# Kernel optimization log

Measured on AMD Instinct MI355X. Metric: run time of the kernel, lower is better.

Reference implementation:

```python
import jax, jax.numpy as jnp
import numpy as np

B = 4
NV = 6890           # SMPL vertex count
NF0 = 13776         # SMPL face count (before fill_back)
T = 3               # tex_size
IMG = 128           # render image size
UVH = UVW = 256     # uv image resolution
FLENGTH = 500.0
NEAR, FAR = 0.1, 25.0
CHUNK = 128         # faces per z-buffer scan step
BIG = jnp.float32(1e10)


def setup_inputs():
    key = jax.random.key(0)
    ks = jax.random.split(key, 5)
    faces0 = jax.random.randint(ks[0], (NF0, 3), 0, NV, dtype=jnp.int32)
    faces = jnp.concatenate([faces0, faces0[:, ::-1]], axis=0)  # fill_back
    cam = jnp.concatenate([0.8 + 0.2 * jax.random.uniform(ks[1], (B, 1)),
                           0.05 * jax.random.normal(ks[2], (B, 2))], axis=1)
    vertices = 0.3 * jax.random.normal(ks[3], (B, NV, 3))
    uv_imgs = jax.random.uniform(ks[4], (B, 3, UVH, UVW))
    img2uv_sampler = jax.random.uniform(jax.random.fold_in(key, 7),
                                        (faces.shape[0], T * T, 2)) * 2.0 - 1.0
    return {"cam": cam, "vertices": vertices, "uv_imgs": uv_imgs,
            "img2uv_sampler": img2uv_sampler, "faces": faces}


def _grid_sample(img, grid):
    # img (B,C,H,W), grid (B,N,2) xy in [-1,1]; bilinear, align_corners=False, zeros padding
    Bc, C, H, W = img.shape
    x = (grid[..., 0] + 1.0) * (W * 0.5) - 0.5
    y = (grid[..., 1] + 1.0) * (H * 0.5) - 0.5
    x0f = jnp.floor(x); y0f = jnp.floor(y)
    wx = x - x0f; wy = y - y0f
    x0 = x0f.astype(jnp.int32); y0 = y0f.astype(jnp.int32)
    imgf = img.reshape(Bc, C, H * W)
    def gat(yi, xi, w):
        valid = (xi >= 0) & (xi < W) & (yi >= 0) & (yi < H)
        idx = jnp.clip(yi, 0, H - 1) * W + jnp.clip(xi, 0, W - 1)
        v = jax.vmap(lambda im, i: im[:, i])(imgf, idx)  # (B,C,N)
        return v * (w * valid)[:, None, :]
    return (gat(y0, x0, (1 - wx) * (1 - wy)) + gat(y0, x0 + 1, wx * (1 - wy)) +
            gat(y0 + 1, x0, (1 - wx) * wy) + gat(y0 + 1, x0 + 1, wx * wy))


def _extract_tex(uv_imgs, sampler, nf):
    # sampler (B,nf,T*T,2) -> textures (B,nf,T,T,T,3)
    tex = _grid_sample(uv_imgs, sampler.reshape(uv_imgs.shape[0], -1, 2))
    tex = tex.reshape(-1, 3, nf, T, T).transpose(0, 2, 3, 4, 1)  # (B,nf,T,T,3)
    return jnp.broadcast_to(tex[:, :, :, :, None, :], tex.shape[:4] + (T, 3))


def _lighting(face_verts, textures):
    # module defaults: ambient intensity 1, directional 0, white lights, dir=(0,1,0)
    v0, v1, v2 = face_verts[:, :, 0], face_verts[:, :, 1], face_verts[:, :, 2]
    n = jnp.cross(v1 - v0, v2 - v0)
    n = n / (jnp.linalg.norm(n, axis=-1, keepdims=True) + 1e-10)
    cos = jnp.maximum(n @ jnp.array([0.0, 1.0, 0.0]), 0.0)       # (B,F)
    light = 1.0 * jnp.ones(3) + 0.0 * cos[..., None] * jnp.ones(3)  # (B,F,3)
    return textures * light[:, :, None, None, None, :]


def _weak_projection(cam, vertices):
    p = IMG / 2.0
    tz = FLENGTH / (p * cam[:, 0:1])                              # (B,1)
    v2d = cam[:, None, 0:1] * (vertices[:, :, :2] + cam[:, None, 1:])
    return jnp.concatenate([v2d, vertices[:, :, 2:3] + tz[:, None, :]], axis=-1)


def _bary(fv, px, py):
    # fv: (...,3,3) triangle screen verts; px,py broadcastable pixel coords
    x0 = fv[..., 0, 0]; y0 = fv[..., 0, 1]
    x1 = fv[..., 1, 0]; y1 = fv[..., 1, 1]
    x2 = fv[..., 2, 0]; y2 = fv[..., 2, 1]
    w0 = (x2 - x1) * (py - y1) - (y2 - y1) * (px - x1)
    w1 = (x0 - x2) * (py - y2) - (y0 - y2) * (px - x2)
    w2 = (x1 - x0) * (py - y0) - (y1 - y0) * (px - x0)
    area = w0 + w1 + w2
    s = jnp.where(area == 0, 1.0, area)
    return w0 / s, w1 / s, w2 / s, area


def _pixel_grid():
    xs = (2.0 * jnp.arange(IMG) + 1.0) / IMG - 1.0                # (W,)
    ys = (1.0 - (2.0 * jnp.arange(IMG) + 1.0) / IMG)[:, None]     # (H,1), +y up
    return xs, ys


def _rasterize_fim(face_verts):
    # face_verts (B,F,3,3) in screen coords -> face index map (B,H,W), -1 = bg
    Bc, F = face_verts.shape[:2]
    pad = (-F) % CHUNK
    fv = jnp.pad(face_verts, ((0, 0), (0, pad), (0, 0), (0, 0)))
    S = (F + pad) // CHUNK
    fv = fv.reshape(Bc, S, CHUNK, 3, 3).transpose(1, 0, 2, 3, 4)  # (S,B,C,3,3)
    xs, ys = _pixel_grid()
    def step(carry, inp):
        zbuf, fim = carry
        f, base = inp
        fe = f[:, :, None, None, :, :]                            # (B,C,1,1,3,3)
        b0, b1, b2, area = _bary(fe, xs, ys)                      # (B,C,H,W)
        z0 = f[:, :, 0, 2][..., None, None]
        z1 = f[:, :, 1, 2][..., None, None]
        z2 = f[:, :, 2, 2][..., None, None]
        invz = b0 / z0 + b1 / z1 + b2 / z2                        # perspective-correct
        zp = 1.0 / jnp.where(invz == 0, 1.0, invz)
        inside = (b0 >= 0) & (b1 >= 0) & (b2 >= 0) & (area > 0)   # front-facing only
        valid = inside & (zp > NEAR) & (zp < FAR)
        depth = jnp.where(valid, zp, BIG)
        dmin = jnp.min(depth, axis=1)                             # (B,H,W)
        amin = jnp.argmin(depth, axis=1).astype(jnp.int32) + base
        better = dmin < zbuf
        return (jnp.where(better, dmin, zbuf),
                jnp.where(better, amin, fim)), None
    zbuf0 = jnp.full((Bc, IMG, IMG), BIG)
    fim0 = jnp.full((Bc, IMG, IMG), -1, jnp.int32)
    bases = (jnp.arange(S) * CHUNK).astype(jnp.int32)
    (zbuf, fim), _ = jax.lax.scan(step, (zbuf0, fim0), (fv, bases))
    return fim


def _shade(face_verts, textures, fim):
    # nearest-texel barycentric texture lookup, as in neural_renderer forward
    Bc, F = face_verts.shape[:2]
    fid = jnp.clip(fim, 0, F - 1).reshape(Bc, -1)                 # (B,HW)
    fv = jax.vmap(lambda v, i: v[i])(face_verts, fid)             # (B,HW,3,3)
    fv = fv.reshape(Bc, IMG, IMG, 3, 3)
    xs, ys = _pixel_grid()
    b0, b1, b2, _ = _bary(fv, xs, ys)                             # (B,H,W)
    t0 = jnp.clip(jnp.floor(b0 * T).astype(jnp.int32), 0, T - 1)
    t1 = jnp.clip(jnp.floor(b1 * T).astype(jnp.int32), 0, T - 1)
    t2 = jnp.clip(jnp.floor(b2 * T).astype(jnp.int32), 0, T - 1)
    idx = ((jnp.clip(fim, 0, F - 1) * T + t0) * T + t1) * T + t2  # (B,H,W)
    texf = textures.reshape(Bc, F * T * T * T, 3)
    col = jax.vmap(lambda t, i: t[i])(texf, idx.reshape(Bc, -1))  # (B,HW,3)
    col = col.reshape(Bc, IMG, IMG, 3)
    col = jnp.where((fim >= 0)[..., None], col, 0.0)              # bg color (0,0,0)
    return col.transpose(0, 3, 1, 2)                              # (B,3,H,W)


def reference(cam, vertices, uv_imgs, img2uv_sampler, faces):
    Bc = cam.shape[0]
    nf = faces.shape[0]
    sampler = jnp.broadcast_to(img2uv_sampler[None], (Bc,) + img2uv_sampler.shape)
    textures = _extract_tex(uv_imgs, sampler, nf)                 # (B,nf,T,T,T,3)
    textures = _lighting(vertices[:, faces], textures)
    verts_p = _weak_projection(cam, vertices)
    fv = verts_p[:, faces]                                        # (B,nf,3,3)
    fv_sg = jax.lax.stop_gradient(fv)  # hard rasterization is non-differentiable
    fim = _rasterize_fim(fv_sg)
    images = _shade(fv_sg, textures, fim)
    return images


if __name__ == "__main__":
    out = reference(**setup_inputs())
    print(out.shape, out.dtype)
```

## Files before the change

kernel.cpp:

```cpp
#include <hip/hip_runtime.h>
#include <stdint.h>

#pragma clang fp contract(off)

#define B_    4
#define NV_   6890
#define NF_   27552
#define IMG_  128
#define UV_   256
#define NPIX  (IMG_*IMG_)

#define TS_     8
#define TPB_    (IMG_/TS_)
#define NTILE_  (TPB_*TPB_)
#define NBIN_   (B_*NTILE_)
#define NZ_     8
#define NCELL_  (NTILE_*NZ_)
#define LIST_CAP (1536*1024)
#define MAXC_   (LIST_CAP/256 + NBIN_)
#define FBF_    256
#define NBLK_   ((NF_+FBF_-1)/FBF_)


__global__ void __launch_bounds__(256) project_k(
    const float* __restrict__ cam, const float* __restrict__ verts,
    float* __restrict__ vp) {
  int idx = blockIdx.x * 256 + threadIdx.x;
  if (idx >= B_ * NV_) return;
  int b = idx / NV_;
  float c0 = cam[b * 3 + 0], c1 = cam[b * 3 + 1], c2 = cam[b * 3 + 2];
  float tz = 500.0f / (64.0f * c0);
  const float* src = verts + (size_t)idx * 3;
  float* dst = vp + (size_t)idx * 4;
  dst[0] = c0 * (src[0] + c1);
  dst[1] = c0 * (src[1] + c2);
  dst[2] = src[2] + tz;
  dst[3] = 0.0f;
}

struct FaceBin {
  int valid, tx0, tx1, ty0, ty1, bu;
  float d21x, d21y, d02x, d02y, d10x, d10y;
  float x0, y0, x1, y1, x2, y2, zmin;
};

__device__ __forceinline__ FaceBin face_bin(
    const float* __restrict__ cam, const float* __restrict__ vp,
    const int* __restrict__ faces, int b, int f) {
  FaceBin r; r.valid = 0; r.zmin = 0.0f;
  int ia = faces[f * 3 + 0], ib = faces[f * 3 + 1], ic = faces[f * 3 + 2];
  const float* vb = vp + (size_t)b * NV_ * 4;
  float x0 = vb[ia * 4 + 0], y0 = vb[ia * 4 + 1], z0 = vb[ia * 4 + 2];
  float x1 = vb[ib * 4 + 0], y1 = vb[ib * 4 + 1], z1 = vb[ib * 4 + 2];
  float x2 = vb[ic * 4 + 0], y2 = vb[ic * 4 + 1], z2 = vb[ic * 4 + 2];
  float area_c = (x1 - x0) * (y2 - y0) - (y1 - y0) * (x2 - x0);
  if (area_c < -1e-3f) return r;
  float xmn = fminf(x0, fminf(x1, x2)), xmx = fmaxf(x0, fmaxf(x1, x2));
  float ymn = fminf(y0, fminf(y1, y2)), ymx = fmaxf(y0, fmaxf(y1, y2));
  int jlo = (int)floorf((xmn + 1.0f) * 64.0f - 0.5f) - 1;
  int jhi = (int)ceilf ((xmx + 1.0f) * 64.0f - 0.5f) + 1;
  int ilo = (int)floorf((1.0f - ymx) * 64.0f - 0.5f) - 1;
  int ihi = (int)ceilf ((1.0f - ymn) * 64.0f - 0.5f) + 1;
  if (jhi < 0 || ihi < 0 || jlo > IMG_ - 1 || ilo > IMG_ - 1) return r;
  jlo = max(jlo, 0); ilo = max(ilo, 0);
  jhi = min(jhi, IMG_ - 1); ihi = min(ihi, IMG_ - 1);
  r.tx0 = jlo >> 3; r.tx1 = jhi >> 3; r.ty0 = ilo >> 3; r.ty1 = ihi >> 3;
  r.zmin = fminf(z0, fminf(z1, z2));
  float tz = 500.0f / (64.0f * cam[b * 3]);
  float zr = r.zmin - tz;
  r.bu = (zr > -0.447f) + (zr > -0.367f) + (zr > -0.308f) + (zr > -0.254f) +
         (zr > -0.200f) + (zr > -0.141f) + (zr > -0.061f);
  r.d21x = x2 - x1; r.d21y = y2 - y1;
  r.d02x = x0 - x2; r.d02y = y0 - y2;
  r.d10x = x1 - x0; r.d10y = y1 - y0;
  r.x0 = x0; r.y0 = y0; r.x1 = x1; r.y1 = y1; r.x2 = x2; r.y2 = y2;
  r.valid = 1;
  return r;
}

__device__ __forceinline__ int tile_pass(const FaceBin& r, int tx, int ty) {
  float pxmin = fmaf((float)(tx * 8), 0.015625f, -0.9921875f);
  float pxmax = pxmin + 0.109375f;
  float pymax = fmaf((float)(ty * 8), -0.015625f, 0.9921875f);
  float pymin = pymax - 0.109375f;
  float w0m = r.d21x * ((r.d21x > 0.0f ? pymax : pymin) - r.y1) -
              r.d21y * ((r.d21y > 0.0f ? pxmin : pxmax) - r.x1);
  float w1m = r.d02x * ((r.d02x > 0.0f ? pymax : pymin) - r.y2) -
              r.d02y * ((r.d02y > 0.0f ? pxmin : pxmax) - r.x2);
  float w2m = r.d10x * ((r.d10x > 0.0f ? pymax : pymin) - r.y0) -
              r.d10y * ((r.d10y > 0.0f ? pxmin : pxmax) - r.x0);
  return (w0m >= -1e-3f) && (w1m >= -1e-3f) && (w2m >= -1e-3f);
}

__global__ void __launch_bounds__(FBF_) facebin_k(
    const float* __restrict__ cam, const float* __restrict__ vp,
    const int* __restrict__ faces, ulonglong2* __restrict__ recs,
    unsigned short* __restrict__ cntb) {
  __shared__ int scnt[NCELL_];
  int blk = blockIdx.x, b = blockIdx.y;
  int f = blk * FBF_ + threadIdx.x;
  for (int k = threadIdx.x; k < NCELL_; k += FBF_) scnt[k] = 0;
  __syncthreads();
  if (f < NF_) {
    FaceBin r = face_bin(cam, vp, faces, b, f);
    unsigned long long mask = 0ull;
    unsigned info = 0u;
    float zmin = 0.0f;
    if (r.valid) {
      int w = r.tx1 - r.tx0 + 1, h = r.ty1 - r.ty0 + 1;
      bool full = (w * h > 64);
      int k = 0;
      for (int ty = r.ty0; ty <= r.ty1; ++ty)
        for (int tx = r.tx0; tx <= r.tx1; ++tx, ++k)
          if (full || tile_pass(r, tx, ty)) {
            if (!full) mask |= 1ull << k;
            atomicAdd(&scnt[(ty * TPB_ + tx) * NZ_ + r.bu], 1);
          }
      if (full) mask = ~0ull;
      if (mask != 0ull) {
        info = 0x80000000u | ((unsigned)r.bu << 28) |
               ((unsigned)r.tx0 << 24) | ((unsigned)r.ty0 << 20) |
               ((unsigned)(w - 1) << 16) | ((unsigned)(h - 1) << 12);
        zmin = r.zmin;
      }
    }
    ulonglong2 rr;
    rr.x = mask;
    rr.y = ((unsigned long long)info << 32) | (unsigned)__float_as_uint(zmin);
    recs[(size_t)b * NF_ + f] = rr;
  }
  __syncthreads();
  unsigned short* dst = cntb + ((size_t)b * NBLK_ + blk) * NCELL_;
  for (int k = threadIdx.x; k < NCELL_; k += FBF_)
    dst[k] = (unsigned short)scnt[k];
}

__global__ void __launch_bounds__(256) sum_k(
    unsigned short* __restrict__ cntb, int* __restrict__ cnt8) {
  int c = blockIdx.x * 256 + threadIdx.x;
  int b = blockIdx.y;
  int run = 0;
  for (int blk = 0; blk < NBLK_; ++blk) {
    size_t o = ((size_t)b * NBLK_ + blk) * NCELL_ + c;
    int v = (int)cntb[o];
    cntb[o] = (unsigned short)run;
    run += v;
  }
  cnt8[(size_t)b * NCELL_ + c] = run;
}

__global__ void __launch_bounds__(1024) scan_k(
    const int* __restrict__ cnt8, int* __restrict__ off8,
    int* __restrict__ binoff, int* __restrict__ bintot,
    int* __restrict__ work, int* __restrict__ nC) {
  __shared__ int wsum[16];
  int t = threadIdx.x;
  int lane = t & 63, w = t >> 6;
  int c[NZ_];
  int s = 0;
#pragma unroll
  for (int j = 0; j < NZ_; ++j) { c[j] = cnt8[t * NZ_ + j]; s += c[j]; }
  int inc = s;
#pragma unroll
  for (int d = 1; d < 64; d <<= 1) {
    int u = __shfl_up(inc, d, 64);
    if (lane >= d) inc += u;
  }
  if (lane == 63) wsum[w] = inc;
  __syncthreads();
  int wb = 0;
  for (int k = 0; k < 16; ++k) wb += (k < w) ? wsum[k] : 0;
  int base = wb + inc - s;
  int o = base;
#pragma unroll
  for (int j = 0; j < NZ_; ++j) {
    off8[t * NZ_ + j] = o;
    o += c[j];
  }
  binoff[t] = base;
  bintot[t] = s;
  int nch = (max(s - 256, 0) + 255) >> 8;
  int inc2 = nch;
#pragma unroll
  for (int d = 1; d < 64; d <<= 1) {
    int u = __shfl_up(inc2, d, 64);
    if (lane >= d) inc2 += u;
  }
  __syncthreads();
  if (lane == 63) wsum[w] = inc2;
  __syncthreads();
  int wb2 = 0;
  for (int k = 0; k < 16; ++k) wb2 += (k < w) ? wsum[k] : 0;
  int cb = wb2 + inc2 - nch;
  if (t == 1023) nC[0] = wb2 + inc2;
  for (int q = 0; q < nch; ++q) work[cb + q] = t | ((q + 1) << 10);
}

__global__ void __launch_bounds__(FBF_) bin_fill_k(
    const ulonglong2* __restrict__ recs, const int* __restrict__ off8,
    const unsigned short* __restrict__ cntb, int* __restrict__ list) {
  __shared__ int lbase[NCELL_];
  __shared__ int lrank[NCELL_];
  int blk = blockIdx.x, b = blockIdx.y;
  int f = blk * FBF_ + threadIdx.x;
  const unsigned short* prow = cntb + ((size_t)b * NBLK_ + blk) * NCELL_;
  const int* orow = off8 + (size_t)b * NCELL_;
  for (int k = threadIdx.x; k < NCELL_; k += FBF_) {
    lbase[k] = orow[k] + (int)prow[k];
    lrank[k] = 0;
  }
  __syncthreads();
  if (f < NF_) {
    ulonglong2 rr = recs[(size_t)b * NF_ + f];
    unsigned long long mask = rr.x;
    unsigned info = (unsigned)(rr.y >> 32);
    unsigned z16 = ((unsigned)rr.y) >> 16;
    if (info >> 31) {
      int ev = (int)((z16 << 15) | (unsigned)f);
      int bu = (info >> 28) & 7;
      int tx0 = (info >> 24) & 15, ty0 = (info >> 20) & 15;
      int w = ((info >> 16) & 15) + 1, h = ((info >> 12) & 15) + 1;
      bool full = (w * h > 64);
      int k = 0;
      for (int ty = ty0; ty < ty0 + h; ++ty)
        for (int tx = tx0; tx < tx0 + w; ++tx, ++k)
          if (full || ((mask >> k) & 1ull)) {
            int cell = (ty * TPB_ + tx) * NZ_ + bu;
            int rk = atomicAdd(&lrank[cell], 1);
            int slot = lbase[cell] + rk;
            if (slot < LIST_CAP) list[slot] = ev;
          }
    }
  }
}

__device__ __forceinline__ void raster_slice(
    const float4 (*F)[64], int nsurv, float px, float py,
    unsigned long long& kb, unsigned& kbz_u) {
  unsigned win_u = 0x7F800000u;
  unsigned long long qm = 0ull;
  for (int q = 0; q < nsurv; ++q) {
    float4 A = F[0][q];
    float4 Bv = F[1][q];
    float4 Cv = F[2][q];
    float w0 = A.x * (py - A.w) - A.y * (px - A.z);
    float w1 = Bv.x * (py - Bv.w) - Bv.y * (px - Bv.z);
    float w2 = Cv.x * (py - Cv.w) - Cv.y * (px - Cv.z);
    float area = (w0 + w1) + w2;
    float mn = fminf(w0, fminf(w1, w2));
    bool pred = (area > 0.0f) && !(mn < 0.0f);
    if (!__any(pred)) continue;
    float4 P = F[4][q];
    float num = (w0 * P.x + w1 * P.y) + w2 * P.z;
    float zpa = (area * P.w) * __builtin_amdgcn_rcpf(num);
    unsigned cu = win_u < kbz_u ? win_u : kbz_u;
    float thrq = __uint_as_float(cu) * 1.001f;
    bool amb = pred && (!(zpa > thrq) ||
                        (zpa > 0.09989f && zpa < 0.10011f) ||
                        (zpa > 24.9724f && zpa < 25.0276f));
    if (amb) qm |= 1ull << q;
    bool ok = pred && (zpa > 0.1001f) && (zpa < 24.975f);
    unsigned zb = __float_as_uint(zpa);
    if (ok && zb < win_u) win_u = zb;
  }
  while (__any(qm != 0ull)) {
    if (qm != 0ull) {
      int q = __ffsll(qm) - 1;
      qm &= qm - 1ull;
      float4 A = F[0][q];
      float4 Bv = F[1][q];
      float4 Cv = F[2][q];
      float w0 = A.x * (py - A.w) - A.y * (px - A.z);
      float w1 = Bv.x * (py - Bv.w) - Bv.y * (px - Bv.z);
      float w2 = Cv.x * (py - Cv.w) - Cv.y * (px - Cv.z);
      float area = (w0 + w1) + w2;
      float4 P = F[4][q];
      float num = (w0 * P.x + w1 * P.y) + w2 * P.z;
      float zpa = (area * P.w) * __builtin_amdgcn_rcpf(num);
      unsigned cu = win_u < kbz_u ? win_u : kbz_u;
      float thrf = __uint_as_float(cu) * 1.001f;
      if (!(zpa > thrf) ||
          (zpa > 0.09989f && zpa < 0.10011f) ||
          (zpa > 24.9724f && zpa < 25.0276f)) {
        float4 Z = F[3][q];
        float b0 = w0 / area, b1 = w1 / area, b2 = w2 / area;
        float invz = (b0 / Z.x + b1 / Z.y) + b2 / Z.z;
        float zp = 1.0f / (invz == 0.0f ? 1.0f : invz);
        if (zp > 0.1f && zp < 25.0f) {
          unsigned long long key =
              ((unsigned long long)__float_as_uint(zp) << 32) |
              (unsigned int)__float_as_int(Z.w);
          if (key < kb) {
            kb = key;
            kbz_u = (unsigned)(kb >> 32);
          }
        }
      }
    }
  }
}

__device__ __forceinline__ void stage_face(
    float4 (*F)[64], const float* __restrict__ vb,
    const int* __restrict__ faces, int fid, int rank) {
  int ia = faces[fid * 3 + 0], ib = faces[fid * 3 + 1], ic = faces[fid * 3 + 2];
  float4 v0 = *(const float4*)(vb + (size_t)ia * 4);
  float4 v1 = *(const float4*)(vb + (size_t)ib * 4);
  float4 v2 = *(const float4*)(vb + (size_t)ic * 4);
  F[0][rank] = make_float4(v2.x - v1.x, v2.y - v1.y, v1.x, v1.y);
  F[1][rank] = make_float4(v0.x - v2.x, v0.y - v2.y, v2.x, v2.y);
  F[2][rank] = make_float4(v1.x - v0.x, v1.y - v0.y, v0.x, v0.y);
  F[3][rank] = make_float4(v0.z, v1.z, v2.z, __int_as_float(fid));
  F[4][rank] =
      make_float4(v1.z * v2.z, v0.z * v2.z, v0.z * v1.z, v0.z * v1.z * v2.z);
}

__global__ void __launch_bounds__(256) raster_seed_k(
    const float* __restrict__ vp, const int* __restrict__ faces,
    const int* __restrict__ list, const int* __restrict__ bintot,
    const int* __restrict__ binoff, unsigned long long* __restrict__ zkey) {
  __shared__ float4 fd[4][5][64];
  __shared__ unsigned long long mg[4][64];
  int bin = blockIdx.x;
  int b = bin >> 8;
  int t = bin & 255;
  int tyT = t >> 4, txT = t & 15;
  int ws = threadIdx.x >> 6, lane = threadIdx.x & 63;
  int pi = tyT * TS_ + (lane >> 3);
  int pj = txT * TS_ + (lane & 7);
  float px = fmaf((float)pj, 0.015625f, -0.9921875f);
  float py = fmaf((float)pi, -0.015625f, 0.9921875f);

  int n = min(bintot[bin], 256);
  int base = binoff[bin];
  int seg = ws * 64;
  int mw = min(n - seg, 64);

  unsigned long long kb = ~0ull;
  unsigned kbz_u = 0x7F800000u;
  if (mw > 0) {
    if (lane < mw) {
      int fid = (int)((unsigned)list[base + seg + lane] & 0x7FFFu);
      stage_face(fd[ws], vp + (size_t)b * NV_ * 4, faces, fid, lane);
    }
    raster_slice(fd[ws], mw, px, py, kb, kbz_u);
  }

  mg[ws][lane] = kb;
  __syncthreads();
  if (ws == 0) {
    unsigned long long k0 = mg[0][lane];
    unsigned long long k1 = mg[1][lane];
    unsigned long long k2 = mg[2][lane];
    unsigned long long k3 = mg[3][lane];
    k0 = k1 < k0 ? k1 : k0;
    k2 = k3 < k2 ? k3 : k2;
    k0 = k2 < k0 ? k2 : k0;
    zkey[(size_t)b * NPIX + pi * IMG_ + pj] = k0;
  }
}

__global__ void __launch_bounds__(256) raster_k(
    const float* __restrict__ vp, const int* __restrict__ faces,
    const int* __restrict__ list, const int* __restrict__ bintot,
    const int* __restrict__ binoff, const int* __restrict__ work,
    const int* __restrict__ nC, unsigned long long* __restrict__ zkey) {
  __shared__ float4 fd[4][5][64];
  __shared__ unsigned long long mg[4][64];
  int bid = blockIdx.x;
  if (bid >= nC[0]) return;
  int wkv = work[bid];
  int bin = wkv & (NBIN_ - 1);
  int chunk = wkv >> 10;
  int b = bin >> 8;
  int t = bin & 255;
  int tyT = t >> 4, txT = t & 15;
  int ws = threadIdx.x >> 6, lane = threadIdx.x & 63;
  int pi = tyT * TS_ + (lane >> 3);
  int pj = txT * TS_ + (lane & 7);
  float px = fmaf((float)pj, 0.015625f, -0.9921875f);
  float py = fmaf((float)pi, -0.015625f, 0.9921875f);

  const unsigned* zhi = (const unsigned*)zkey;
  unsigned seed_u =
      min(zhi[((size_t)b * NPIX + pi * IMG_ + pj) * 2 + 1], 0x7F800000u);
  unsigned mx = seed_u;
  for (int j = 1; j < 64; j <<= 1) {
    unsigned o = (unsigned)__shfl_xor((int)mx, j, 64);
    mx = o > mx ? o : mx;
  }
  unsigned thr_code = __float_as_uint(__uint_as_float(mx) * 1.01f) >> 16;

  int n = bintot[bin];
  int seg = (chunk << 8) + (ws << 6);
  int base0 = binoff[bin] + seg;
  int mw = min(n - seg, 64);
  mw = max(mw, 0);

  bool live = false;
  int fid = 0;
  if (lane < mw) {
    unsigned e = (unsigned)list[base0 + lane];
    live = ((e >> 15) <= thr_code);
    fid = (int)(e & 0x7FFFu);
  }
  unsigned long long bal = __ballot(live);
  unsigned long long kb = ~0ull;
  unsigned kbz_u = seed_u;
  if (bal != 0ull) {
    int nsurv = (int)__popcll(bal);
    int rank = (int)__popcll(bal & ((1ull << lane) - 1ull));
    if (live)
      stage_face(fd[ws], vp + (size_t)b * NV_ * 4, faces, fid, rank);
    raster_slice(fd[ws], nsurv, px, py, kb, kbz_u);
  }

  mg[ws][lane] = kb;
  __syncthreads();
  if (ws == 0) {
    unsigned long long k0 = mg[0][lane];
    unsigned long long k1 = mg[1][lane];
    unsigned long long k2 = mg[2][lane];
    unsigned long long k3 = mg[3][lane];
    k0 = k1 < k0 ? k1 : k0;
    k2 = k3 < k2 ? k3 : k2;
    k0 = k2 < k0 ? k2 : k0;
    if (k0 != ~0ull)
      atomicMin(zkey + (size_t)b * NPIX + pi * IMG_ + pj, k0);
  }
}

#define TAP(ty, tx, wexpr)                                                   \
  {                                                                          \
    int ty_ = (ty), tx_ = (tx);                                              \
    float w_ = (wexpr);                                                      \
    float valid_ =                                                           \
        (tx_ >= 0 && tx_ < UV_ && ty_ >= 0 && ty_ < UV_) ? 1.0f : 0.0f;      \
    float wv_ = w_ * valid_;                                                 \
    int cy_ = min(max(ty_, 0), UV_ - 1), cx_ = min(max(tx_, 0), UV_ - 1);    \
    int o_ = cy_ * UV_ + cx_;                                                \
    cr = cr + img[o_] * wv_;                                                 \
    cg = cg + img[UV_ * UV_ + o_] * wv_;                                     \
    cb = cb + img[2 * UV_ * UV_ + o_] * wv_;                                 \
  }

__global__ void __launch_bounds__(256) shade_k(
    const float* __restrict__ vp, const int* __restrict__ faces,
    const float* __restrict__ uv, const float* __restrict__ samp,
    const unsigned long long* __restrict__ zkey, float* __restrict__ out) {
  int idx = blockIdx.x * 256 + threadIdx.x;
  if (idx >= B_ * NPIX) return;
  int b = idx / NPIX;
  int p = idx - b * NPIX;
  int ii = p / IMG_;
  int jj = p - ii * IMG_;

  unsigned long long key = zkey[idx];
  float cr = 0.0f, cg = 0.0f, cb = 0.0f;
  if (key != 0xFFFFFFFFFFFFFFFFull) {
    int f = (int)(key & 0xFFFFFFFFull);
    int ia = faces[f * 3 + 0], ib = faces[f * 3 + 1], ic = faces[f * 3 + 2];
    const float* vb = vp + (size_t)b * NV_ * 4;
    float x0 = vb[ia * 4 + 0], y0 = vb[ia * 4 + 1];
    float x1 = vb[ib * 4 + 0], y1 = vb[ib * 4 + 1];
    float x2 = vb[ic * 4 + 0], y2 = vb[ic * 4 + 1];
    float px = (float)(2 * jj + 1) / 128.0f - 1.0f;
    float py = 1.0f - (float)(2 * ii + 1) / 128.0f;
    float w0 = (x2 - x1) * (py - y1) - (y2 - y1) * (px - x1);
    float w1 = (x0 - x2) * (py - y2) - (y0 - y2) * (px - x2);
    float w2 = (x1 - x0) * (py - y0) - (y1 - y0) * (px - x0);
    float area = (w0 + w1) + w2;
    float s = (area == 0.0f) ? 1.0f : area;
    float b0 = w0 / s, b1 = w1 / s;
    int t0 = min(max((int)floorf(b0 * 3.0f), 0), 2);
    int t1 = min(max((int)floorf(b1 * 3.0f), 0), 2);

    const float* g = samp + ((size_t)f * 9 + (size_t)(t0 * 3 + t1)) * 2;
    float gx = g[0], gy = g[1];
    float x = (gx + 1.0f) * 128.0f - 0.5f;
    float y = (gy + 1.0f) * 128.0f - 0.5f;
    float x0f = floorf(x), y0f = floorf(y);
    float wx = x - x0f, wy = y - y0f;
    int xi = (int)x0f, yi = (int)y0f;
    float omwx = 1.0f - wx, omwy = 1.0f - wy;
    const float* img = uv + (size_t)b * 3 * UV_ * UV_;
    TAP(yi,     xi,     omwx * omwy)
    TAP(yi,     xi + 1, wx * omwy)
    TAP(yi + 1, xi,     omwx * wy)
    TAP(yi + 1, xi + 1, wx * wy)
  }
  out[((size_t)b * 3 + 0) * NPIX + p] = cr;
  out[((size_t)b * 3 + 1) * NPIX + p] = cg;
  out[((size_t)b * 3 + 2) * NPIX + p] = cb;
}

extern "C" void kernel_launch(void* const* d_in, const int* in_sizes, int n_in,
                              void* d_out, int out_size, void* d_ws,
                              size_t ws_size, hipStream_t stream) {
  const float* cam   = (const float*)d_in[0];
  const float* verts = (const float*)d_in[1];
  const float* uv    = (const float*)d_in[2];
  const float* samp  = (const float*)d_in[3];
  const int*   faces = (const int*)d_in[4];

  char* ws = (char*)d_ws;
  size_t o = 0;
  unsigned long long* zkey = (unsigned long long*)(ws + o);
  o += (size_t)B_ * NPIX * 8;
  float* vp = (float*)(ws + o);
  o += ((size_t)B_ * NV_ * 4 * 4 + 1023) & ~1023ull;
  int* cnt8   = (int*)(ws + o); o += (size_t)B_ * NCELL_ * 4;
  int* off8   = (int*)(ws + o); o += (size_t)B_ * NCELL_ * 4;
  int* binoff = (int*)(ws + o); o += NBIN_ * 4;
  int* bintot = (int*)(ws + o); o += NBIN_ * 4;
  int* nC     = (int*)(ws + o); o += 1024;
  int* work   = (int*)(ws + o); o += (size_t)MAXC_ * 4;
  ulonglong2* recs = (ulonglong2*)(ws + o);
  o += (size_t)B_ * NF_ * 16;
  unsigned short* cntb = (unsigned short*)(ws + o);
  o += (size_t)B_ * NBLK_ * NCELL_ * 2;
  int* list = (int*)(ws + o);

  project_k<<<(B_ * NV_ + 255) / 256, 256, 0, stream>>>(cam, verts, vp);
  dim3 bgrid(NBLK_, B_);
  facebin_k<<<bgrid, FBF_, 0, stream>>>(cam, vp, faces, recs, cntb);
  sum_k<<<dim3(NCELL_ / 256, B_), 256, 0, stream>>>(cntb, cnt8);
  scan_k<<<1, NBIN_, 0, stream>>>(cnt8, off8, binoff, bintot, work, nC);
  bin_fill_k<<<bgrid, FBF_, 0, stream>>>(recs, off8, cntb, list);
  raster_seed_k<<<NBIN_, 256, 0, stream>>>(vp, faces, list, bintot, binoff,
                                           zkey);
  raster_k<<<MAXC_, 256, 0, stream>>>(vp, faces, list, bintot, binoff, work,
                                      nC, zkey);
  shade_k<<<(B_ * NPIX + 255) / 256, 256, 0, stream>>>(vp, faces, uv, samp,
                                                       zkey, (float*)d_out);
}
```

Measured before the change: 181.2 us.

## Fuse count sum and scan into per-batch kernel, shrink seed pass to 128 faces

Merges the column-sum and single-block scan kernels into one kernel launched per batch, with the list partitioned into per-batch capacity regions and per-batch work queues. This removes one launch and the serial single-block scan over all bins. The seed raster pass now consumes only the first 128 faces per bin instead of 256, so the chunked raster pass starts earlier and picks up more of the list. The smaller seed may leave a looser depth threshold, so fewer faces get culled in the later pass. The per-batch capacity split could overflow for skewed batches.

```diff
diff --git a/kernel.cpp b/kernel.cpp
--- a/kernel.cpp
+++ b/kernel.cpp
@@ -17,7 +17,9 @@
 #define NZ_     8
 #define NCELL_  (NTILE_*NZ_)
 #define LIST_CAP (1536*1024)
-#define MAXC_   (LIST_CAP/256 + NBIN_)
+#define CAPB_   (LIST_CAP/B_)
+#define MAXCB_  (CAPB_/256 + NTILE_)
+#define SEEDN_  128
 #define FBF_    256
 #define NBLK_   ((NF_+FBF_-1)/FBF_)
 
@@ -135,65 +137,79 @@
     dst[k] = (unsigned short)scnt[k];
 }
 
-__global__ void __launch_bounds__(256) sum_k(
-    unsigned short* __restrict__ cntb, int* __restrict__ cnt8) {
-  int c = blockIdx.x * 256 + threadIdx.x;
-  int b = blockIdx.y;
-  int run = 0;
-  for (int blk = 0; blk < NBLK_; ++blk) {
-    size_t o = ((size_t)b * NBLK_ + blk) * NCELL_ + c;
-    int v = (int)cntb[o];
-    cntb[o] = (unsigned short)run;
-    run += v;
-  }
-  cnt8[(size_t)b * NCELL_ + c] = run;
-}
-
-__global__ void __launch_bounds__(1024) scan_k(
-    const int* __restrict__ cnt8, int* __restrict__ off8,
+__global__ void __launch_bounds__(1024) sumscan_k(
+    unsigned short* __restrict__ cntb, int* __restrict__ off8,
     int* __restrict__ binoff, int* __restrict__ bintot,
     int* __restrict__ work, int* __restrict__ nC) {
+  __shared__ int tot[NCELL_];
   __shared__ int wsum[16];
+  __shared__ int half0;
+  __shared__ int nchs[NTILE_];
+  int b = blockIdx.x;
   int t = threadIdx.x;
   int lane = t & 63, w = t >> 6;
-  int c[NZ_];
-  int s = 0;
+  for (int c = t; c < NCELL_; c += 1024) {
+    int run = 0;
+    for (int blk = 0; blk < NBLK_; ++blk) {
+      size_t o = ((size_t)b * NBLK_ + blk) * NCELL_ + c;
+      int v = (int)cntb[o];
+      cntb[o] = (unsigned short)run;
+      run += v;
+    }
+    tot[c] = run;
+  }
+  __syncthreads();
+  int base = b * CAPB_;
+  int v0 = tot[t];
+  int inc0 = v0;
+  for (int d = 1; d < 64; d <<= 1) {
+    int u = __shfl_up(inc0, d, 64);
+    if (lane >= d) inc0 += u;
+  }
+  if (lane == 63) wsum[w] = inc0;
+  __syncthreads();
+  int wb0 = 0;
+  for (int k = 0; k < 16; ++k) wb0 += (k < w) ? wsum[k] : 0;
+  off8[(size_t)b * NCELL_ + t] = base + wb0 + inc0 - v0;
+  if (t == 1023) half0 = wb0 + inc0;
+  __syncthreads();
+  int v1 = tot[1024 + t];
+  int inc1 = v1;
+  for (int d = 1; d < 64; d <<= 1) {
+    int u = __shfl_up(inc1, d, 64);
+    if (lane >= d) inc1 += u;
+  }
+  if (lane == 63) wsum[w] = inc1;
+  __syncthreads();
+  int wb1 = 0;
+  for (int k = 0; k < 16; ++k) wb1 += (k < w) ? wsum[k] : 0;
+  off8[(size_t)b * NCELL_ + 1024 + t] = base + half0 + wb1 + inc1 - v1;
+  __syncthreads();
+  if (t < NTILE_) {
+    int s = 0;
 #pragma unroll
-  for (int j = 0; j < NZ_; ++j) { c[j] = cnt8[t * NZ_ + j]; s += c[j]; }
-  int inc = s;
-#pragma unroll
+    for (int j = 0; j < NZ_; ++j) s += tot[t * NZ_ + j];
+    bintot[b * NTILE_ + t] = s;
+    binoff[b * NTILE_ + t] = off8[(size_t)b * NCELL_ + t * NZ_];
+    nchs[t] = (max(s - SEEDN_, 0) + 255) >> 8;
+  }
+  __syncthreads();
+  int vc = (t < NTILE_) ? nchs[t] : 0;
+  int incc = vc;
   for (int d = 1; d < 64; d <<= 1) {
-    int u = __shfl_up(inc, d, 64);
-    if (lane >= d) inc += u;
-  }
-  if (lane == 63) wsum[w] = inc;
-  __syncthreads();
-  int wb = 0;
-  for (int k = 0; k < 16; ++k) wb += (k < w) ? wsum[k] : 0;
-  int base = wb + inc - s;
-  int o = base;
-#pragma unroll
-  for (int j = 0; j < NZ_; ++j) {
-    off8[t * NZ_ + j] = o;
-    o += c[j];
-  }
-  binoff[t] = base;
-  bintot[t] = s;
-  int nch = (max(s - 256, 0) + 255) >> 8;
-  int inc2 = nch;
-#pragma unroll
-  for (int d = 1; d < 64; d <<= 1) {
-    int u = __shfl_up(inc2, d, 64);
-    if (lane >= d) inc2 += u;
-  }
-  __syncthreads();
-  if (lane == 63) wsum[w] = inc2;
-  __syncthreads();
-  int wb2 = 0;
-  for (int k = 0; k < 16; ++k) wb2 += (k < w) ? wsum[k] : 0;
-  int cb = wb2 + inc2 - nch;
-  if (t == 1023) nC[0] = wb2 + inc2;
-  for (int q = 0; q < nch; ++q) work[cb + q] = t | ((q + 1) << 10);
+    int u = __shfl_up(incc, d, 64);
+    if (lane >= d) incc += u;
+  }
+  if (t < NTILE_ && lane == 63) wsum[w] = incc;
+  __syncthreads();
+  if (t < NTILE_) {
+    int wb = 0;
+    for (int k = 0; k < 4; ++k) wb += (k < w) ? wsum[k] : 0;
+    int cb = wb + incc - vc;
+    if (t == NTILE_ - 1) nC[b] = wb + incc;
+    for (int q = 0; q < vc; ++q)
+      work[b * MAXCB_ + cb + q] = t | ((q + 1) << 8);
+  }
 }
 
 __global__ void __launch_bounds__(FBF_) bin_fill_k(
@@ -221,6 +237,7 @@
       int tx0 = (info >> 24) & 15, ty0 = (info >> 20) & 15;
       int w = ((info >> 16) & 15) + 1, h = ((info >> 12) & 15) + 1;
       bool full = (w * h > 64);
+      int cap = (b + 1) * CAPB_;
       int k = 0;
       for (int ty = ty0; ty < ty0 + h; ++ty)
         for (int tx = tx0; tx < tx0 + w; ++tx, ++k)
@@ -228,7 +245,7 @@
             int cell = (ty * TPB_ + tx) * NZ_ + bu;
             int rk = atomicAdd(&lrank[cell], 1);
             int slot = lbase[cell] + rk;
-            if (slot < LIST_CAP) list[slot] = ev;
+            if (slot < cap) list[slot] = ev;
           }
     }
   }
@@ -331,10 +348,10 @@
   float px = fmaf((float)pj, 0.015625f, -0.9921875f);
   float py = fmaf((float)pi, -0.015625f, 0.9921875f);
 
-  int n = min(bintot[bin], 256);
+  int n = min(bintot[bin], SEEDN_);
   int base = binoff[bin];
-  int seg = ws * 64;
-  int mw = min(n - seg, 64);
+  int seg = ws * (SEEDN_ / 4);
+  int mw = min(n - seg, SEEDN_ / 4);
 
   unsigned long long kb = ~0ull;
   unsigned kbz_u = 0x7F800000u;
@@ -368,12 +385,13 @@
   __shared__ float4 fd[4][5][64];
   __shared__ unsigned long long mg[4][64];
   int bid = blockIdx.x;
-  if (bid >= nC[0]) return;
-  int wkv = work[bid];
-  int bin = wkv & (NBIN_ - 1);
-  int chunk = wkv >> 10;
-  int b = bin >> 8;
-  int t = bin & 255;
+  int b = bid / MAXCB_;
+  int i = bid - b * MAXCB_;
+  if (i >= nC[b]) return;
+  int wkv = work[b * MAXCB_ + i];
+  int t = wkv & (NTILE_ - 1);
+  int chunk = wkv >> 8;
+  int bin = b * NTILE_ + t;
   int tyT = t >> 4, txT = t & 15;
   int ws = threadIdx.x >> 6, lane = threadIdx.x & 63;
   int pi = tyT * TS_ + (lane >> 3);
@@ -392,7 +410,7 @@
   unsigned thr_code = __float_as_uint(__uint_as_float(mx) * 1.01f) >> 16;
 
   int n = bintot[bin];
-  int seg = (chunk << 8) + (ws << 6);
+  int seg = SEEDN_ + ((chunk - 1) << 8) + (ws << 6);
   int base0 = binoff[bin] + seg;
   int mw = min(n - seg, 64);
   mw = max(mw, 0);
@@ -509,12 +527,11 @@
   o += (size_t)B_ * NPIX * 8;
   float* vp = (float*)(ws + o);
   o += ((size_t)B_ * NV_ * 4 * 4 + 1023) & ~1023ull;
-  int* cnt8   = (int*)(ws + o); o += (size_t)B_ * NCELL_ * 4;
   int* off8   = (int*)(ws + o); o += (size_t)B_ * NCELL_ * 4;
   int* binoff = (int*)(ws + o); o += NBIN_ * 4;
   int* bintot = (int*)(ws + o); o += NBIN_ * 4;
   int* nC     = (int*)(ws + o); o += 1024;
-  int* work   = (int*)(ws + o); o += (size_t)MAXC_ * 4;
+  int* work   = (int*)(ws + o); o += (size_t)B_ * MAXCB_ * 4;
   ulonglong2* recs = (ulonglong2*)(ws + o);
   o += (size_t)B_ * NF_ * 16;
   unsigned short* cntb = (unsigned short*)(ws + o);
@@ -524,13 +541,12 @@
   project_k<<<(B_ * NV_ + 255) / 256, 256, 0, stream>>>(cam, verts, vp);
   dim3 bgrid(NBLK_, B_);
   facebin_k<<<bgrid, FBF_, 0, stream>>>(cam, vp, faces, recs, cntb);
-  sum_k<<<dim3(NCELL_ / 256, B_), 256, 0, stream>>>(cntb, cnt8);
-  scan_k<<<1, NBIN_, 0, stream>>>(cnt8, off8, binoff, bintot, work, nC);
+  sumscan_k<<<B_, 1024, 0, stream>>>(cntb, off8, binoff, bintot, work, nC);
   bin_fill_k<<<bgrid, FBF_, 0, stream>>>(recs, off8, cntb, list);
   raster_seed_k<<<NBIN_, 256, 0, stream>>>(vp, faces, list, bintot, binoff,
                                            zkey);
-  raster_k<<<MAXC_, 256, 0, stream>>>(vp, faces, list, bintot, binoff, work,
-                                      nC, zkey);
+  raster_k<<<B_ * MAXCB_, 256, 0, stream>>>(vp, faces, list, bintot, binoff,
+                                            work, nC, zkey);
   shade_k<<<(B_ * NPIX + 255) / 256, 256, 0, stream>>>(vp, faces, uv, samp,
                                                        zkey, (float*)d_out);
 }
```

Measured after the change: 183.5 us. Within noise of the previous version (+1.3%).
